# Optimization experiments

Hardware: AMD Instinct MI355X
Metric: run time of the kernel (lower is better)

Reference implementation:

```python
import jax, jax.numpy as jnp
import numpy as np

B, HS, WS = 4, 64, 64
UP = 8
H, W = HS * UP, WS * UP
C_ORI, C_MNT, C_OFF = 90, 180, 8
K = 1024            # max minutiae candidates per image (64*64 cells max 4096)
THRESH = 0.5
DIST_T = 16.0
ANG_T = np.pi / 6


def setup_inputs() -> dict:
    key = jax.random.key(0)
    ks = jax.random.split(key, 8)
    return {
        'segmentation': jax.random.uniform(ks[0], (B, 1, HS, WS), jnp.float32),
        'segmentation_up': jax.random.uniform(ks[1], (B, 1, H, W), jnp.float32),
        'orientation_up': jax.random.normal(ks[2], (B, C_ORI, H, W), jnp.float32),
        'enhanced_real': jax.random.normal(ks[3], (B, 1, H, W), jnp.float32),
        'minutiae_score': jax.random.uniform(ks[4], (B, 1, HS, WS), jnp.float32),
        'minutiae_orientation': jax.random.normal(ks[5], (B, C_MNT, HS, WS), jnp.float32),
        'minutiae_x_offset': jax.random.normal(ks[6], (B, C_OFF, HS, WS), jnp.float32),
        'minutiae_y_offset': jax.random.normal(ks[7], (B, C_OFF, HS, WS), jnp.float32),
    }


def _opening(x, k):
    # morphological opening (erosion then dilation) with a k x k ones kernel,
    # separable min/max pooling; geodesic border (pad so border is neutral).
    pl, pr = (k - 1) // 2, k // 2

    def pool(v, comp, init, pad_val):
        vp = jnp.pad(v, ((0, 0), (pl, pr), (pl, pr)), constant_values=pad_val)
        vp = jax.lax.reduce_window(vp, init, comp, (1, k, 1), (1, 1, 1), 'VALID')
        return jax.lax.reduce_window(vp, init, comp, (1, 1, k), (1, 1, 1), 'VALID')

    er = pool(x, jax.lax.min, np.inf, 1e4)
    return pool(er, jax.lax.max, -np.inf, -1e4)


def _nms_keep(xy, ang, valid):
    # xy: [K,2], ang: [K], valid: [K] bool; entries already sorted by score desc
    d = jnp.sqrt(jnp.sum((xy[:, None, :] - xy[None, :, :]) ** 2, axis=-1))
    da = jnp.abs(ang[:, None] - ang[None, :])
    da = jnp.minimum(da, 2 * jnp.pi - da)
    sup = (d < DIST_T) & (da < ANG_T) & valid[:, None] & valid[None, :]
    idxs = jnp.arange(K)

    def body(i, keep):
        return keep & ~(sup[i] & (idxs > i) & keep[i])

    return jax.lax.fori_loop(0, K, body, valid)


def _detect(score, ori, xo, yo):
    # score: [HS,WS]; ori: [C_MNT,HS,WS]; xo/yo: [C_OFF,HS,WS]
    h, w = score.shape
    flat = score.reshape(-1)
    masked = jnp.where(flat > THRESH, flat, -1.0)
    vals, idx = jax.lax.top_k(masked, K)          # sorted descending
    valid = vals > THRESH
    rows = idx // w
    cols = idx % w
    ang_idx = jnp.argmax(ori.reshape(C_MNT, -1)[:, idx], axis=0)
    xoff = jnp.argmax(xo.reshape(C_OFF, -1)[:, idx], axis=0)
    yoff = jnp.argmax(yo.reshape(C_OFF, -1)[:, idx], axis=0)
    angles = (ang_idx.astype(jnp.float32) * 2.0 - 89.0) * (np.pi / 180.0)
    xc = cols.astype(jnp.float32) * 8.0 + xoff.astype(jnp.float32)
    yc = rows.astype(jnp.float32) * 8.0 + yoff.astype(jnp.float32)
    scores = flat[idx]
    m = jnp.stack([xc, yc, angles, scores], axis=-1)  # [K,4]
    keep = _nms_keep(m[:, :2], angles, valid)
    return m, keep


def reference(segmentation, segmentation_up, orientation_up, enhanced_real,
              minutiae_score, minutiae_orientation, minutiae_x_offset,
              minutiae_y_offset):
    mask = _opening(jnp.round(segmentation[:, 0]), 5)          # [B,HS,WS]
    mask_up = _opening(jnp.round(segmentation_up[:, 0]), 5 * UP)  # [B,H,W]

    score = minutiae_score[:, 0] * mask
    minut, keep = jax.vmap(_detect)(score, minutiae_orientation,
                                    minutiae_x_offset, minutiae_y_offset)
    minut = minut * keep[..., None].astype(minut.dtype)       # zero suppressed

    ori_field = (jnp.argmax(orientation_up, axis=1).astype(jnp.float32) * 2.0
                 - 90.0) * (np.pi / 180.0) * mask_up

    enh = enhanced_real[:, 0] * mask_up
    ef = enh.reshape(B, -1)
    emin = ef.min(axis=1, keepdims=True)
    emax = ef.max(axis=1, keepdims=True)
    enh_vis = ((ef - emin) / (emax - emin + 1e-8)).reshape(B, H, W) * 255.0

    return (minut, keep.astype(jnp.float32), enh_vis, mask_up * 255.0, ori_field)
```

## Files before the change

kernel.cpp:

```cpp
#include <hip/hip_runtime.h>
#include <math.h>

#define HSd 64
#define WSd 64
#define Hh 512
#define Wh 512
#define Bn 4
#define C_ORIc 90
#define C_MNTc 180
#define C_OFFc 8
#define Kc 1024

#define O_MINUT 0
#define O_KEEP  (Bn*Kc*4)
#define O_VIS   (O_KEEP + Bn*Kc)
#define O_MASK  (O_VIS + Bn*Hh*Wh)
#define O_ORI   (O_MASK + Bn*Hh*Wh)

#define PI_180 0.017453292519943295f
#define TWO_PI 6.283185307179586f
#define ANG_T  0.5235987755982988f

__global__ __launch_bounds__(256) void small_mask_kernel(const float* __restrict__ seg,
                                                         float* __restrict__ mask_out)
{
    __shared__ float a[64][65];
    __shared__ float t[64][65];
    int b = blockIdx.x;
    const float* s = seg + b * 4096;
    for (int i = threadIdx.x; i < 4096; i += 256)
        a[i >> 6][i & 63] = rintf(s[i]);
    __syncthreads();
    for (int i = threadIdx.x; i < 4096; i += 256) {
        int r = i >> 6, c = i & 63;
        int lo = max(r - 2, 0), hi = min(r + 2, 63);
        float m = 1e30f;
        for (int rr = lo; rr <= hi; rr++) m = fminf(m, a[rr][c]);
        t[r][c] = m;
    }
    __syncthreads();
    for (int i = threadIdx.x; i < 4096; i += 256) {
        int r = i >> 6, c = i & 63;
        int lo = max(c - 2, 0), hi = min(c + 2, 63);
        float m = 1e30f;
        for (int cc = lo; cc <= hi; cc++) m = fminf(m, t[r][cc]);
        a[r][c] = m;
    }
    __syncthreads();
    for (int i = threadIdx.x; i < 4096; i += 256) {
        int r = i >> 6, c = i & 63;
        int lo = max(r - 2, 0), hi = min(r + 2, 63);
        float m = -1e30f;
        for (int rr = lo; rr <= hi; rr++) m = fmaxf(m, a[rr][c]);
        t[r][c] = m;
    }
    __syncthreads();
    for (int i = threadIdx.x; i < 4096; i += 256) {
        int r = i >> 6, c = i & 63;
        int lo = max(c - 2, 0), hi = min(c + 2, 63);
        float m = -1e30f;
        for (int cc = lo; cc <= hi; cc++) m = fmaxf(m, t[r][cc]);
        mask_out[b * 4096 + i] = m;
    }
}

template <bool ISMIN, bool BIN>
__global__ __launch_bounds__(256) void pass_v(const float* __restrict__ in,
                                              float* __restrict__ out)
{
    int c = blockIdx.x * 64 + threadIdx.x;
    int r = blockIdx.y * 4 + threadIdx.y;
    int b = blockIdx.z;
    const float* p = in + (size_t)b * Hh * Wh;
    int lo = max(r - 19, 0), hi = min(r + 20, Hh - 1);
    float acc = ISMIN ? 1e30f : -1e30f;
    for (int rr = lo; rr <= hi; rr++) {
        float v = p[rr * Wh + c];
        if (BIN) v = rintf(v);
        acc = ISMIN ? fminf(acc, v) : fmaxf(acc, v);
    }
    out[(size_t)b * Hh * Wh + (size_t)r * Wh + c] = acc;
}

template <bool ISMIN>
__global__ __launch_bounds__(256) void pass_h(const float* __restrict__ in,
                                              float* __restrict__ out)
{
    int c = blockIdx.x * 64 + threadIdx.x;
    int r = blockIdx.y * 4 + threadIdx.y;
    int b = blockIdx.z;
    const float* p = in + (size_t)b * Hh * Wh + (size_t)r * Wh;
    int lo = max(c - 19, 0), hi = min(c + 20, Wh - 1);
    float acc = ISMIN ? 1e30f : -1e30f;
    for (int cc = lo; cc <= hi; cc++)
        acc = ISMIN ? fminf(acc, p[cc]) : fmaxf(acc, p[cc]);
    out[(size_t)b * Hh * Wh + (size_t)r * Wh + c] = acc;
}

__global__ __launch_bounds__(512) void final_up_kernel(const float* __restrict__ vmx,
                                                       const float* __restrict__ ori,
                                                       const float* __restrict__ enh,
                                                       float* __restrict__ out,
                                                       float* __restrict__ partials)
{
    int r = blockIdx.x, b = blockIdx.y, c = threadIdx.x;
    __shared__ float row[512];
    __shared__ float rmn[512];
    __shared__ float rmx[512];
    size_t base = (size_t)b * Hh * Wh + (size_t)r * Wh;
    row[c] = vmx[base + c];
    __syncthreads();
    int lo = max(c - 19, 0), hi = min(c + 20, Wh - 1);
    float m = -1e30f;
    for (int cc = lo; cc <= hi; cc++) m = fmaxf(m, row[cc]);
    out[O_MASK + base + c] = m * 255.0f;

    float of = 0.0f;
    if (m != 0.0f) {
        const float* op = ori + (size_t)b * C_ORIc * Hh * Wh + (size_t)r * Wh + c;
        float best = op[0];
        int bi = 0;
        for (int ch = 1; ch < C_ORIc; ch++) {
            float v = op[(size_t)ch * Hh * Wh];
            if (v > best) { best = v; bi = ch; }
        }
        of = ((float)bi * 2.0f - 90.0f) * PI_180 * m;
    }
    out[O_ORI + base + c] = of;

    float e = enh[base + c] * m;
    rmn[c] = e; rmx[c] = e;
    __syncthreads();
    for (int s2 = 256; s2 > 0; s2 >>= 1) {
        if (c < s2) {
            rmn[c] = fminf(rmn[c], rmn[c + s2]);
            rmx[c] = fmaxf(rmx[c], rmx[c + s2]);
        }
        __syncthreads();
    }
    if (c == 0) {
        partials[(b * Hh + r) * 2 + 0] = rmn[0];
        partials[(b * Hh + r) * 2 + 1] = rmx[0];
    }
}

__global__ __launch_bounds__(512) void reduce_mm_kernel(const float* __restrict__ partials,
                                                        float* __restrict__ mm)
{
    int b = blockIdx.x, t = threadIdx.x;
    __shared__ float mn[512];
    __shared__ float mx[512];
    mn[t] = partials[(b * 512 + t) * 2 + 0];
    mx[t] = partials[(b * 512 + t) * 2 + 1];
    __syncthreads();
    for (int s = 256; s > 0; s >>= 1) {
        if (t < s) {
            mn[t] = fminf(mn[t], mn[t + s]);
            mx[t] = fmaxf(mx[t], mx[t + s]);
        }
        __syncthreads();
    }
    if (t == 0) { mm[b * 2] = mn[0]; mm[b * 2 + 1] = mx[0]; }
}

__global__ __launch_bounds__(256) void vis_kernel(const float* __restrict__ enh,
                                                  const float* __restrict__ maskout,
                                                  const float* __restrict__ mm,
                                                  float* __restrict__ vis)
{
    int idx = blockIdx.x * 256 + threadIdx.x;
    int b = idx >> 18;
    float m = (maskout[idx] != 0.0f) ? 1.0f : 0.0f;
    float e = enh[idx] * m;
    float emin = mm[b * 2], emax = mm[b * 2 + 1];
    float r = (e - emin) / (emax - emin + 1e-8f);
    vis[idx] = r * 255.0f;
}

__global__ __launch_bounds__(1024) void detect_kernel(const float* __restrict__ mscore,
                                                      const float* __restrict__ maskS,
                                                      const float* __restrict__ mo,
                                                      const float* __restrict__ xo,
                                                      const float* __restrict__ yo,
                                                      float* __restrict__ out)
{
    int b = blockIdx.x;
    int tid = threadIdx.x;
    __shared__ unsigned long long keys[4096];
    __shared__ float sx[1024];
    __shared__ float sy[1024];
    __shared__ float sa[1024];
    __shared__ int keep[1024];

    const float* sp = mscore + b * 4096;
    const float* mp = maskS + b * 4096;
    for (int i = tid; i < 4096; i += 1024) {
        float s = sp[i] * mp[i];
        float mval = (s > 0.5f) ? s : -1.0f;
        unsigned int fb = __float_as_uint(mval);
        unsigned int od = (fb & 0x80000000u) ? ~fb : (fb | 0x80000000u);
        keys[i] = ((unsigned long long)(~od) << 32) | (unsigned int)i;
    }
    for (int k = 2; k <= 4096; k <<= 1) {
        for (int j = k >> 1; j > 0; j >>= 1) {
            __syncthreads();
            for (int t = tid; t < 4096; t += 1024) {
                int ixj = t ^ j;
                if (ixj > t) {
                    unsigned long long va = keys[t], vb = keys[ixj];
                    bool up = ((t & k) == 0);
                    if ((va > vb) == up) { keys[t] = vb; keys[ixj] = va; }
                }
            }
        }
    }
    __syncthreads();

    int idx = (int)(keys[tid] & 0xffffffffu);
    float s = sp[idx] * mp[idx];
    bool valid = s > 0.5f;
    int Nv = __syncthreads_count(valid);

    float xc = 0.f, yc = 0.f, ang = 0.f;
    if (tid < Nv) {
        int rr = idx >> 6, cc = idx & 63;
        const float* op = mo + (size_t)b * C_MNTc * 4096 + idx;
        float best = op[0]; int bi = 0;
        for (int ch = 1; ch < C_MNTc; ch++) {
            float v = op[ch * 4096];
            if (v > best) { best = v; bi = ch; }
        }
        const float* xp = xo + (size_t)b * C_OFFc * 4096 + idx;
        float bxv = xp[0]; int bx = 0;
        for (int ch = 1; ch < C_OFFc; ch++) {
            float v = xp[ch * 4096];
            if (v > bxv) { bxv = v; bx = ch; }
        }
        const float* yp = yo + (size_t)b * C_OFFc * 4096 + idx;
        float byv = yp[0]; int by = 0;
        for (int ch = 1; ch < C_OFFc; ch++) {
            float v = yp[ch * 4096];
            if (v > byv) { byv = v; by = ch; }
        }
        ang = ((float)bi * 2.0f - 89.0f) * PI_180;
        xc = (float)cc * 8.0f + (float)bx;
        yc = (float)rr * 8.0f + (float)by;
        sx[tid] = xc; sy[tid] = yc; sa[tid] = ang;
        keep[tid] = 1;
    } else {
        keep[tid] = 0;
    }
    __syncthreads();

    for (int i = 0; i < Nv; i++) {
        if (keep[i] && tid > i && tid < Nv && keep[tid]) {
            float dx = sx[tid] - sx[i], dy = sy[tid] - sy[i];
            float d = sqrtf(dx * dx + dy * dy);
            float da = fabsf(sa[tid] - sa[i]);
            da = fminf(da, TWO_PI - da);
            if (d < 16.0f && da < ANG_T) keep[tid] = 0;
        }
        __syncthreads();
    }

    int kf = keep[tid];
    float* mout = out + O_MINUT + (size_t)b * Kc * 4 + (size_t)tid * 4;
    if (kf) {
        mout[0] = xc; mout[1] = yc; mout[2] = ang; mout[3] = s;
    } else {
        mout[0] = 0.f; mout[1] = 0.f; mout[2] = 0.f; mout[3] = 0.f;
    }
    out[O_KEEP + b * Kc + tid] = (float)kf;
}

extern "C" void kernel_launch(void* const* d_in, const int* in_sizes, int n_in,
                              void* d_out_, int out_size, void* d_ws, size_t ws_size,
                              hipStream_t stream)
{
    const float* seg    = (const float*)d_in[0];
    const float* segup  = (const float*)d_in[1];
    const float* oriup  = (const float*)d_in[2];
    const float* enh    = (const float*)d_in[3];
    const float* mscore = (const float*)d_in[4];
    const float* mori   = (const float*)d_in[5];
    const float* mxo    = (const float*)d_in[6];
    const float* myo    = (const float*)d_in[7];
    float* out = (float*)d_out_;

    float* maskS    = (float*)d_ws;
    float* partials = maskS + Bn * 4096;
    float* mm       = partials + Bn * 512 * 2;

    float* T1 = out + O_VIS;
    float* T2 = out + O_ORI;

    small_mask_kernel<<<Bn, 256, 0, stream>>>(seg, maskS);
    detect_kernel<<<Bn, 1024, 0, stream>>>(mscore, maskS, mori, mxo, myo, out);

    dim3 pb(64, 4);
    dim3 pg(8, 128, Bn);
    pass_v<true, true><<<pg, pb, 0, stream>>>(segup, T1);
    pass_h<true><<<pg, pb, 0, stream>>>(T1, T2);
    pass_v<false, false><<<pg, pb, 0, stream>>>(T2, T1);
    final_up_kernel<<<dim3(Hh, Bn), 512, 0, stream>>>(T1, oriup, enh, out, partials);
    reduce_mm_kernel<<<Bn, 512, 0, stream>>>(partials, mm);
    vis_kernel<<<(Bn * Hh * Wh) / 256, 256, 0, stream>>>(enh, out + O_MASK, mm, out + O_VIS);
}
```

Before: 579.0 us.

## Fuse low-res mask opening into detect kernel and exit early when no candidates

```diff
diff --git a/kernel.cpp b/kernel.cpp
--- a/kernel.cpp
+++ b/kernel.cpp
@@ -20,49 +20,6 @@
 #define PI_180 0.017453292519943295f
 #define TWO_PI 6.283185307179586f
 #define ANG_T  0.5235987755982988f
-
-__global__ __launch_bounds__(256) void small_mask_kernel(const float* __restrict__ seg,
-                                                         float* __restrict__ mask_out)
-{
-    __shared__ float a[64][65];
-    __shared__ float t[64][65];
-    int b = blockIdx.x;
-    const float* s = seg + b * 4096;
-    for (int i = threadIdx.x; i < 4096; i += 256)
-        a[i >> 6][i & 63] = rintf(s[i]);
-    __syncthreads();
-    for (int i = threadIdx.x; i < 4096; i += 256) {
-        int r = i >> 6, c = i & 63;
-        int lo = max(r - 2, 0), hi = min(r + 2, 63);
-        float m = 1e30f;
-        for (int rr = lo; rr <= hi; rr++) m = fminf(m, a[rr][c]);
-        t[r][c] = m;
-    }
-    __syncthreads();
-    for (int i = threadIdx.x; i < 4096; i += 256) {
-        int r = i >> 6, c = i & 63;
-        int lo = max(c - 2, 0), hi = min(c + 2, 63);
-        float m = 1e30f;
-        for (int cc = lo; cc <= hi; cc++) m = fminf(m, t[r][cc]);
-        a[r][c] = m;
-    }
-    __syncthreads();
-    for (int i = threadIdx.x; i < 4096; i += 256) {
-        int r = i >> 6, c = i & 63;
-        int lo = max(r - 2, 0), hi = min(r + 2, 63);
-        float m = -1e30f;
-        for (int rr = lo; rr <= hi; rr++) m = fmaxf(m, a[rr][c]);
-        t[r][c] = m;
-    }
-    __syncthreads();
-    for (int i = threadIdx.x; i < 4096; i += 256) {
-        int r = i >> 6, c = i & 63;
-        int lo = max(c - 2, 0), hi = min(c + 2, 63);
-        float m = -1e30f;
-        for (int cc = lo; cc <= hi; cc++) m = fmaxf(m, t[r][cc]);
-        mask_out[b * 4096 + i] = m;
-    }
-}
 
 template <bool ISMIN, bool BIN>
 __global__ __launch_bounds__(256) void pass_v(const float* __restrict__ in,
@@ -178,7 +135,7 @@
 }
 
 __global__ __launch_bounds__(1024) void detect_kernel(const float* __restrict__ mscore,
-                                                      const float* __restrict__ maskS,
+                                                      const float* __restrict__ seg,
                                                       const float* __restrict__ mo,
                                                       const float* __restrict__ xo,
                                                       const float* __restrict__ yo,
@@ -187,15 +144,61 @@
     int b = blockIdx.x;
     int tid = threadIdx.x;
     __shared__ unsigned long long keys[4096];
-    __shared__ float sx[1024];
-    __shared__ float sy[1024];
-    __shared__ float sa[1024];
-    __shared__ int keep[1024];
+    __shared__ float maskT[64][65];
+    float* scratch = (float*)keys;
+
+    const float* sg = seg + b * 4096;
+    for (int i = tid; i < 4096; i += 1024)
+        maskT[i >> 6][i & 63] = rintf(sg[i]);
+    __syncthreads();
+    for (int i = tid; i < 4096; i += 1024) {
+        int r = i >> 6, c = i & 63;
+        int lo = max(r - 2, 0), hi = min(r + 2, 63);
+        float m = 1e30f;
+        for (int rr = lo; rr <= hi; rr++) m = fminf(m, maskT[rr][c]);
+        scratch[r * 65 + c] = m;
+    }
+    __syncthreads();
+    for (int i = tid; i < 4096; i += 1024) {
+        int r = i >> 6, c = i & 63;
+        int lo = max(c - 2, 0), hi = min(c + 2, 63);
+        float m = 1e30f;
+        for (int cc = lo; cc <= hi; cc++) m = fminf(m, scratch[r * 65 + cc]);
+        maskT[r][c] = m;
+    }
+    __syncthreads();
+    for (int i = tid; i < 4096; i += 1024) {
+        int r = i >> 6, c = i & 63;
+        int lo = max(r - 2, 0), hi = min(r + 2, 63);
+        float m = -1e30f;
+        for (int rr = lo; rr <= hi; rr++) m = fmaxf(m, maskT[rr][c]);
+        scratch[r * 65 + c] = m;
+    }
+    __syncthreads();
+    for (int i = tid; i < 4096; i += 1024) {
+        int r = i >> 6, c = i & 63;
+        int lo = max(c - 2, 0), hi = min(c + 2, 63);
+        float m = -1e30f;
+        for (int cc = lo; cc <= hi; cc++) m = fmaxf(m, scratch[r * 65 + cc]);
+        maskT[r][c] = m;
+    }
+    __syncthreads();
 
     const float* sp = mscore + b * 4096;
-    const float* mp = maskS + b * 4096;
-    for (int i = tid; i < 4096; i += 1024) {
-        float s = sp[i] * mp[i];
+    bool anyv = false;
+    for (int i = tid; i < 4096; i += 1024) {
+        float s = sp[i] * maskT[i >> 6][i & 63];
+        anyv |= (s > 0.5f);
+    }
+    if (!__syncthreads_or(anyv)) {
+        float* mout = out + O_MINUT + (size_t)b * Kc * 4 + (size_t)tid * 4;
+        mout[0] = 0.f; mout[1] = 0.f; mout[2] = 0.f; mout[3] = 0.f;
+        out[O_KEEP + b * Kc + tid] = 0.f;
+        return;
+    }
+
+    for (int i = tid; i < 4096; i += 1024) {
+        float s = sp[i] * maskT[i >> 6][i & 63];
         float mval = (s > 0.5f) ? s : -1.0f;
         unsigned int fb = __float_as_uint(mval);
         unsigned int od = (fb & 0x80000000u) ? ~fb : (fb | 0x80000000u);
@@ -217,9 +220,14 @@
     __syncthreads();
 
     int idx = (int)(keys[tid] & 0xffffffffu);
-    float s = sp[idx] * mp[idx];
+    float s = sp[idx] * maskT[idx >> 6][idx & 63];
     bool valid = s > 0.5f;
     int Nv = __syncthreads_count(valid);
+
+    float* sx = scratch;
+    float* sy = scratch + 1024;
+    float* sa = scratch + 2048;
+    int*   keep = (int*)(scratch + 3072);
 
     float xc = 0.f, yc = 0.f, ang = 0.f;
     if (tid < Nv) {
@@ -287,15 +295,13 @@
     const float* myo    = (const float*)d_in[7];
     float* out = (float*)d_out_;
 
-    float* maskS    = (float*)d_ws;
-    float* partials = maskS + Bn * 4096;
+    float* partials = (float*)d_ws;
     float* mm       = partials + Bn * 512 * 2;
 
     float* T1 = out + O_VIS;
     float* T2 = out + O_ORI;
 
-    small_mask_kernel<<<Bn, 256, 0, stream>>>(seg, maskS);
-    detect_kernel<<<Bn, 1024, 0, stream>>>(mscore, maskS, mori, mxo, myo, out);
+    detect_kernel<<<Bn, 1024, 0, stream>>>(mscore, seg, mori, mxo, myo, out);
 
     dim3 pb(64, 4);
     dim3 pg(8, 128, Bn);
```

Result: faster. 511.8 us (-11.6%).
